# Kernel optimization log

Measured on AMD Instinct MI355X. Metric: run time of the kernel, lower is better.

The kernel has to match this reference:

```python
import jax, jax.numpy as jnp
import numpy as np

MODEL_DIM = 512
NUM_HEADS = 16
D_OUTPUT = 128
DIM_PER_HEAD = MODEL_DIM // NUM_HEADS  # 32
LN_EPS = 1e-5


def setup_inputs() -> dict:
    key = jax.random.key(0)
    ks = jax.random.split(key, 12)
    B = 128
    proj = MODEL_DIM * D_OUTPUT  # 65536
    s = 0.02
    return {
        "key": jax.random.normal(ks[0], (B, 1, MODEL_DIM), jnp.float32),
        "value": jax.random.normal(ks[1], (B, 1, MODEL_DIM), jnp.float32),
        "query": jax.random.normal(ks[2], (B, 1, MODEL_DIM), jnp.float32),
        "Wk": jax.random.normal(ks[3], (MODEL_DIM, proj), jnp.float32) * s,
        "bk": jnp.zeros((proj,), jnp.float32),
        "Wv": jax.random.normal(ks[4], (MODEL_DIM, proj), jnp.float32) * s,
        "bv": jnp.zeros((proj,), jnp.float32),
        "Wq": jax.random.normal(ks[5], (MODEL_DIM, proj), jnp.float32) * s,
        "bq": jnp.zeros((proj,), jnp.float32),
        "Wo": jax.random.normal(ks[6], (MODEL_DIM, MODEL_DIM), jnp.float32) * s,
        "bo": jnp.zeros((MODEL_DIM,), jnp.float32),
        "gamma": jnp.ones((MODEL_DIM,), jnp.float32),
        "beta": jnp.zeros((MODEL_DIM,), jnp.float32),
    }


def reference(key, value, query, Wk, bk, Wv, bv, Wq, bq, Wo, bo, gamma, beta):
    B = key.shape[0]
    residual = query  # [B, 1, model_dim]
    # QKV projections to model_dim*d_output, then view as (B*H, d_output, dim_per_head)
    k = (key @ Wk + bk).reshape(B * NUM_HEADS, -1, DIM_PER_HEAD)
    v = (value @ Wv + bv).reshape(B * NUM_HEADS, -1, DIM_PER_HEAD)
    q = (query @ Wq + bq).reshape(B * NUM_HEADS, -1, DIM_PER_HEAD)
    # faithful to original: scale = (dim_per_head // num_heads) ** -0.5 (int div)
    scale = (DIM_PER_HEAD // NUM_HEADS) ** (-0.5)
    scores = jnp.einsum('bqd,bkd->bqk', q, k) * scale  # [B*H, S, S]
    attn = jax.nn.softmax(scores, axis=2)
    context = jnp.einsum('bqk,bkd->bqd', attn, v)  # [B*H, S, dph]
    context = context.reshape(B, -1, DIM_PER_HEAD * NUM_HEADS)  # [B, d_output, model_dim]
    out = context @ Wo + bo
    x = residual + out  # broadcast [B,1,D] + [B,d_output,D]
    mu = jnp.mean(x, axis=-1, keepdims=True)
    var = jnp.mean(jnp.square(x - mu), axis=-1, keepdims=True)
    out = (x - mu) * jax.lax.rsqrt(var + LN_EPS) * gamma + beta
    return out, attn
```

## Files before the change

kernel.cpp:

```cpp
#include <hip/hip_runtime.h>

typedef unsigned short u16;
typedef unsigned int u32;
typedef __attribute__((ext_vector_type(4))) float f32x4;
typedef __attribute__((ext_vector_type(4))) u16 u16x4;
typedef __attribute__((ext_vector_type(8))) u16 u16x8;
typedef __attribute__((ext_vector_type(8))) __bf16 bf16x8;

#define DEV static __device__ __forceinline__

DEV u16 f2b(float f) {
  u32 u = __builtin_bit_cast(u32, f);
  u32 r = (u + 0x7fffu + ((u >> 16) & 1u)) >> 16;
  return (u16)r;
}

DEV bf16x8 mk8(u16x4 lo, u16x4 hi) {
  u16x8 v = __builtin_shufflevector(lo, hi, 0, 1, 2, 3, 4, 5, 6, 7);
  return __builtin_bit_cast(bf16x8, v);
}

__global__ __launch_bounds__(256) void prep_x(
    const float* __restrict__ key, const float* __restrict__ value,
    const float* __restrict__ query, u16* __restrict__ Xb)
{
  int idx = blockIdx.x * 256 + threadIdx.x;
  int mat = idx >> 14;
  int off = (idx & 16383) * 4;
  const float* src = mat == 0 ? key : (mat == 1 ? value : query);
  f32x4 v = *(const f32x4*)(src + off);
  u16x4 o;
#pragma unroll
  for (int i = 0; i < 4; ++i) o[i] = __builtin_bit_cast(u16, (__bf16)v[i]);
  *(u16x4*)(Xb + mat * 65536 + off) = o;
}

__global__ __launch_bounds__(256, 3) void qkv_gemm(
    const u16* __restrict__ Xb,
    const float* __restrict__ Wk, const float* __restrict__ bk,
    const float* __restrict__ Wv, const float* __restrict__ bv,
    const float* __restrict__ Wq, const float* __restrict__ bq,
    u16* __restrict__ Kp, u16* __restrict__ Vp, u16* __restrict__ Qp)
{
  const int bx = blockIdx.x;
  const int mat = bx >> 9;
  const float* W    = mat == 0 ? Wk : (mat == 1 ? Wv : Wq);
  const float* bias = mat == 0 ? bk : (mat == 1 ? bv : bq);
  u16* out          = mat == 0 ? Kp : (mat == 1 ? Vp : Qp);
  const u16* Xm = Xb + mat * 65536;
  const int n0 = (bx & 511) * 128;

  __shared__ float Bs[2][32 * 128];
  __shared__ u16   As[2][128 * 32];

  const int t0 = threadIdx.x, lane = t0 & 63, wv = t0 >> 6;
  const int wm = wv >> 1, wn = wv & 1;
  const int l15 = lane & 15, lg = lane >> 4;

  const int brow = wv * 8 + (lane >> 5);
  const int bcol = (lane & 31) * 4;

  f32x4 acc[4][4];
#pragma unroll
  for (int i = 0; i < 4; ++i)
#pragma unroll
    for (int j = 0; j < 4; ++j) acc[i][j] = (f32x4){0.f, 0.f, 0.f, 0.f};

  {
    f32x4 rB[4];
#pragma unroll
    for (int p = 0; p < 4; ++p) {
      int row = brow + p * 2;
      rB[p] = *(const f32x4*)(W + (size_t)row * 65536 + n0 + bcol);
    }
#pragma unroll
    for (int p = 0; p < 2; ++p) {
      int q = wv * 2 + p;
      int m = q * 16 + (lane >> 2);
      int sc = ((lane & 3) - ((m >> 1) & 3)) & 3;
      const u16* gp = Xm + m * 512 + sc * 8;
      u16* lp = &As[0][q * 512];
      __builtin_amdgcn_global_load_lds(
          (const __attribute__((address_space(1))) u32*)gp,
          (__attribute__((address_space(3))) u32*)lp, 16, 0, 0);
    }
#pragma unroll
    for (int p = 0; p < 4; ++p) {
      int row = brow + p * 2;
      int pc = (bcol + (((row >> 3) & 1) << 4)) & 127;
      *(f32x4*)&Bs[0][row * 128 + pc] = rB[p];
    }
    __syncthreads();
  }

  for (int t = 0; t < 16; ++t) {
    const int cur = t & 1, nxt = cur ^ 1;
    f32x4 rB[4];
    if (t < 15) {
      const int k0n = (t + 1) * 32;
#pragma unroll
      for (int p = 0; p < 4; ++p) {
        int row = brow + p * 2;
        rB[p] = *(const f32x4*)(W + (size_t)(k0n + row) * 65536 + n0 + bcol);
      }
#pragma unroll
      for (int p = 0; p < 2; ++p) {
        int q = wv * 2 + p;
        int m = q * 16 + (lane >> 2);
        int sc = ((lane & 3) - ((m >> 1) & 3)) & 3;
        const u16* gp = Xm + m * 512 + k0n + sc * 8;
        u16* lp = &As[nxt][q * 512];
        __builtin_amdgcn_global_load_lds(
            (const __attribute__((address_space(1))) u32*)gp,
            (__attribute__((address_space(3))) u32*)lp, 16, 0, 0);
      }
    }
    __builtin_amdgcn_sched_barrier(0);
    {
      bf16x8 af[4];
#pragma unroll
      for (int mf = 0; mf < 4; ++mf) {
        int m = wm * 64 + mf * 16 + l15;
        af[mf] = *(const bf16x8*)&As[cur][m * 32 + ((lg + ((m >> 1) & 3)) & 3) * 8];
      }
#pragma unroll
      for (int nf = 0; nf < 4; ++nf) {
        int pc = (wn * 64 + nf * 16 + l15 + ((lg & 1) << 4)) & 127;
        bf16x8 bv;
#pragma unroll
        for (int j = 0; j < 8; ++j) bv[j] = (__bf16)Bs[cur][(lg * 8 + j) * 128 + pc];
#pragma unroll
        for (int mf = 0; mf < 4; ++mf)
          acc[mf][nf] = __builtin_amdgcn_mfma_f32_16x16x32_bf16(af[mf], bv, acc[mf][nf], 0, 0, 0);
      }
    }
    __builtin_amdgcn_sched_barrier(0);
    if (t < 15) {
#pragma unroll
      for (int p = 0; p < 4; ++p) {
        int row = brow + p * 2;
        int pc = (bcol + (((row >> 3) & 1) << 4)) & 127;
        *(f32x4*)&Bs[nxt][row * 128 + pc] = rB[p];
      }
    }
    __syncthreads();
  }

  u16* tile = (u16*)&Bs[0][0];
#pragma unroll
  for (int nf = 0; nf < 4; ++nf) {
    int col = wn * 64 + nf * 16 + l15;
    float bv_ = bias[n0 + col];
#pragma unroll
    for (int mf = 0; mf < 4; ++mf) {
      int row0 = wm * 64 + mf * 16 + lg * 4;
#pragma unroll
      for (int r = 0; r < 4; ++r)
        tile[(row0 + r) * 128 + col] = f2b(acc[mf][nf][r] + bv_);
    }
  }
  __syncthreads();
#pragma unroll
  for (int rr = 0; rr < 16; ++rr) {
    int row = wv * 32 + rr * 2 + (lane >> 5);
    int c = (lane & 31) * 4;
    u16x4 v = *(const u16x4*)&tile[row * 128 + c];
    *(u16x4*)(out + (size_t)row * 65536 + n0 + c) = v;
  }
}

__global__ __launch_bounds__(256) void attn_kernel(
    const u16* __restrict__ Qp, const u16* __restrict__ Kp, const u16* __restrict__ Vp,
    float* __restrict__ attnOut, u16* __restrict__ ctx)
{
  const int bh = blockIdx.x;
  const int b = bh >> 4, h = bh & 15;
  const size_t base = (size_t)b * 65536 + h * 4096;

  __shared__ u16 qS[8 * 512];
  __shared__ u16 kS[8 * 512];
  __shared__ u16 vS[32 * 128];
  __shared__ u16 pS[32 * 512];

  const int t = threadIdx.x;
  const int lane = t & 63, w = t >> 6;
  const int l15 = lane & 15, lg = lane >> 4;

#pragma unroll
  for (int p = 0; p < 2; ++p) {
    int idx = p * 256 + t;
    int s = idx >> 2, dc = idx & 3;
    u16x8 qv = *(const u16x8*)(Qp + base + s * 32 + dc * 8);
    u16x8 kv = *(const u16x8*)(Kp + base + s * 32 + dc * 8);
    u16x8 vv = *(const u16x8*)(Vp + base + s * 32 + dc * 8);
    *(u16x4*)(qS + (dc * 2) * 512 + s * 4)     = __builtin_shufflevector(qv, qv, 0, 1, 2, 3);
    *(u16x4*)(qS + (dc * 2 + 1) * 512 + s * 4) = __builtin_shufflevector(qv, qv, 4, 5, 6, 7);
    *(u16x4*)(kS + (dc * 2) * 512 + s * 4)     = __builtin_shufflevector(kv, kv, 0, 1, 2, 3);
    *(u16x4*)(kS + (dc * 2 + 1) * 512 + s * 4) = __builtin_shufflevector(kv, kv, 4, 5, 6, 7);
#pragma unroll
    for (int i = 0; i < 8; ++i)
      vS[(s >> 2) * 128 + (dc * 8 + i) * 4 + (s & 3)] = vv[i];
  }
  __syncthreads();

  f32x4 sc[2][8];
#pragma unroll
  for (int i = 0; i < 2; ++i)
#pragma unroll
    for (int j = 0; j < 8; ++j) sc[i][j] = (f32x4){0.f, 0.f, 0.f, 0.f};

  {
    const int kqA = lg * 2;
    bf16x8 aq[2];
#pragma unroll
    for (int mf = 0; mf < 2; ++mf) {
      int m = w * 32 + mf * 16 + l15;
      u16x4 lo = *(const u16x4*)(qS + kqA * 512 + m * 4);
      u16x4 hi = *(const u16x4*)(qS + (kqA + 1) * 512 + m * 4);
      aq[mf] = mk8(lo, hi);
    }
#pragma unroll
    for (int nf = 0; nf < 8; ++nf) {
      int j = nf * 16 + l15;
      u16x4 lo = *(const u16x4*)(kS + kqA * 512 + j * 4);
      u16x4 hi = *(const u16x4*)(kS + (kqA + 1) * 512 + j * 4);
      bf16x8 bk8 = mk8(lo, hi);
#pragma unroll
      for (int mf = 0; mf < 2; ++mf)
        sc[mf][nf] = __builtin_amdgcn_mfma_f32_16x16x32_bf16(aq[mf], bk8, sc[mf][nf], 0, 0, 0);
    }
  }

  const float SCL = 0.70710678118654752f;
#pragma unroll
  for (int mf = 0; mf < 2; ++mf) {
#pragma unroll
    for (int r = 0; r < 4; ++r) {
      float m8 = -1e30f;
#pragma unroll
      for (int nf = 0; nf < 8; ++nf) m8 = fmaxf(m8, sc[mf][nf][r]);
      m8 = fmaxf(m8, __shfl_xor(m8, 1));
      m8 = fmaxf(m8, __shfl_xor(m8, 2));
      m8 = fmaxf(m8, __shfl_xor(m8, 4));
      m8 = fmaxf(m8, __shfl_xor(m8, 8));
      float s8 = 0.f;
#pragma unroll
      for (int nf = 0; nf < 8; ++nf) {
        float pv = __expf((sc[mf][nf][r] - m8) * SCL);
        sc[mf][nf][r] = pv;
        s8 += pv;
      }
      s8 += __shfl_xor(s8, 1);
      s8 += __shfl_xor(s8, 2);
      s8 += __shfl_xor(s8, 4);
      s8 += __shfl_xor(s8, 8);
      float inv = 1.0f / s8;
      int i = w * 32 + mf * 16 + lg * 4 + r;
      float* ao = attnOut + (size_t)bh * 16384 + (size_t)i * 128;
#pragma unroll
      for (int nf = 0; nf < 8; ++nf) {
        int j = nf * 16 + l15;
        float pv = sc[mf][nf][r] * inv;
        ao[j] = pv;
        pS[(j >> 2) * 512 + i * 4 + (j & 3)] = f2b(pv);
      }
    }
  }
  __syncthreads();

  f32x4 cacc[2][2];
#pragma unroll
  for (int i = 0; i < 2; ++i)
#pragma unroll
    for (int j = 0; j < 2; ++j) cacc[i][j] = (f32x4){0.f, 0.f, 0.f, 0.f};

#pragma unroll
  for (int ks2 = 0; ks2 < 4; ++ks2) {
    const int kqP = ks2 * 8 + lg * 2;
    bf16x8 ap[2];
#pragma unroll
    for (int mf = 0; mf < 2; ++mf) {
      int i = w * 32 + mf * 16 + l15;
      u16x4 lo = *(const u16x4*)(pS + kqP * 512 + i * 4);
      u16x4 hi = *(const u16x4*)(pS + (kqP + 1) * 512 + i * 4);
      ap[mf] = mk8(lo, hi);
    }
#pragma unroll
    for (int nf = 0; nf < 2; ++nf) {
      int d = nf * 16 + l15;
      u16x4 lo = *(const u16x4*)(vS + kqP * 128 + d * 4);
      u16x4 hi = *(const u16x4*)(vS + (kqP + 1) * 128 + d * 4);
      bf16x8 bv8 = mk8(lo, hi);
#pragma unroll
      for (int mf = 0; mf < 2; ++mf)
        cacc[mf][nf] = __builtin_amdgcn_mfma_f32_16x16x32_bf16(ap[mf], bv8, cacc[mf][nf], 0, 0, 0);
    }
  }

  __syncthreads();
#pragma unroll
  for (int mf = 0; mf < 2; ++mf) {
#pragma unroll
    for (int r = 0; r < 4; ++r) {
      int s = w * 32 + mf * 16 + lg * 4 + r;
      int p = s >> 4, q = s & 15;
#pragma unroll
      for (int nf = 0; nf < 2; ++nf) {
        int d = nf * 16 + l15;
        pS[p * 512 + q * 32 + d] = f2b(cacc[mf][nf][r]);
      }
    }
  }
#pragma unroll
  for (int pp = 0; pp < 2; ++pp) {
    int p = w * 2 + pp;
    u16x8 v = *(const u16x8*)&pS[p * 512 + lane * 8];
    *(u16x8*)(ctx + ((size_t)b * 128 + h * 8 + p) * 512 + lane * 8) = v;
  }
}

__global__ __launch_bounds__(256) void out_proj(
    const u16* __restrict__ ctx, const float* __restrict__ Wo, const float* __restrict__ bo,
    const float* __restrict__ query, float* __restrict__ pre)
{
  const int m0 = blockIdx.x * 128;
  const int n0 = blockIdx.y * 128;

  __shared__ u16 As[16 * 512];
  __shared__ u16 Bs[16 * 512];

  const int t = threadIdx.x;
  const int lane = t & 63, wid = t >> 6;
  const int wm = wid >> 1, wn = wid & 1;
  const int l15 = lane & 15, lg = lane >> 4;

  f32x4 acc[4][4];
#pragma unroll
  for (int i = 0; i < 4; ++i)
#pragma unroll
    for (int j = 0; j < 4; ++j) acc[i][j] = (f32x4){0.f, 0.f, 0.f, 0.f};

  for (int it = 0; it < 8; ++it) {
    const int k0 = it * 64;
#pragma unroll
    for (int p = 0; p < 4; ++p) {
      int idx = p * 256 + t;
      int m = idx >> 3, dc = idx & 7;
      u16x8 av = *(const u16x8*)(ctx + (size_t)(m0 + m) * 512 + k0 + dc * 8);
      int kq = dc * 2;
      *(u16x4*)(As + kq * 512 + (((m + 2 * kq) & 127) << 2)) =
          __builtin_shufflevector(av, av, 0, 1, 2, 3);
      *(u16x4*)(As + (kq + 1) * 512 + (((m + 2 * (kq + 1)) & 127) << 2)) =
          __builtin_shufflevector(av, av, 4, 5, 6, 7);
    }
#pragma unroll
    for (int p = 0; p < 8; ++p) {
      int idx = p * 256 + t;
      int n = idx & 127, kq = idx >> 7;
      const float* wp = Wo + (size_t)(k0 + kq * 4) * 512 + n0 + n;
      u16x4 uv;
      uv[0] = f2b(wp[0]);
      uv[1] = f2b(wp[512]);
      uv[2] = f2b(wp[1024]);
      uv[3] = f2b(wp[1536]);
      *(u16x4*)(Bs + kq * 512 + n * 4) = uv;
    }
    __syncthreads();
#pragma unroll
    for (int kstep = 0; kstep < 2; ++kstep) {
      const int kqA = kstep * 8 + lg * 2;
      bf16x8 af[4], bfr[4];
#pragma unroll
      for (int mf = 0; mf < 4; ++mf) {
        int m = wm * 64 + mf * 16 + l15;
        u16x4 lo = *(const u16x4*)(As + kqA * 512 + (((m + 2 * kqA) & 127) << 2));
        u16x4 hi = *(const u16x4*)(As + (kqA + 1) * 512 + (((m + 2 * (kqA + 1)) & 127) << 2));
        af[mf] = mk8(lo, hi);
      }
#pragma unroll
      for (int nf = 0; nf < 4; ++nf) {
        int n = wn * 64 + nf * 16 + l15;
        u16x4 lo = *(const u16x4*)(Bs + kqA * 512 + n * 4);
        u16x4 hi = *(const u16x4*)(Bs + (kqA + 1) * 512 + n * 4);
        bfr[nf] = mk8(lo, hi);
      }
#pragma unroll
      for (int mf = 0; mf < 4; ++mf)
#pragma unroll
        for (int nf = 0; nf < 4; ++nf)
          acc[mf][nf] = __builtin_amdgcn_mfma_f32_16x16x32_bf16(af[mf], bfr[nf], acc[mf][nf], 0, 0, 0);
    }
    __syncthreads();
  }

#pragma unroll
  for (int nf = 0; nf < 4; ++nf) {
    int col = wn * 64 + nf * 16 + l15;
    float bv_ = bo[n0 + col];
#pragma unroll
    for (int mf = 0; mf < 4; ++mf) {
      int row0 = wm * 64 + mf * 16 + lg * 4;
#pragma unroll
      for (int r = 0; r < 4; ++r) {
        int m = m0 + row0 + r;
        float res = query[(m >> 7) * 512 + n0 + col];
        pre[(size_t)m * 512 + n0 + col] = acc[mf][nf][r] + bv_ + res;
      }
    }
  }
}

__global__ __launch_bounds__(256) void ln_kernel(
    const float* __restrict__ pre, const float* __restrict__ gamma,
    const float* __restrict__ beta, float* __restrict__ out0)
{
  const int w = threadIdx.x >> 6, lane = threadIdx.x & 63;
  const int row = blockIdx.x * 4 + w;
  const float* x = pre + (size_t)row * 512;
  f32x4 v0 = *(const f32x4*)(x + lane * 8);
  f32x4 v1 = *(const f32x4*)(x + lane * 8 + 4);
  float s = v0[0] + v0[1] + v0[2] + v0[3] + v1[0] + v1[1] + v1[2] + v1[3];
  float q = v0[0] * v0[0] + v0[1] * v0[1] + v0[2] * v0[2] + v0[3] * v0[3] +
            v1[0] * v1[0] + v1[1] * v1[1] + v1[2] * v1[2] + v1[3] * v1[3];
#pragma unroll
  for (int m = 1; m < 64; m <<= 1) {
    s += __shfl_xor(s, m);
    q += __shfl_xor(q, m);
  }
  float mean = s * (1.f / 512.f);
  float var = q * (1.f / 512.f) - mean * mean;
  float rs = rsqrtf(var + 1e-5f);
  f32x4 g0 = *(const f32x4*)(gamma + lane * 8);
  f32x4 g1 = *(const f32x4*)(gamma + lane * 8 + 4);
  f32x4 b0 = *(const f32x4*)(beta + lane * 8);
  f32x4 b1 = *(const f32x4*)(beta + lane * 8 + 4);
  f32x4 o0, o1;
#pragma unroll
  for (int i = 0; i < 4; ++i) {
    o0[i] = (v0[i] - mean) * rs * g0[i] + b0[i];
    o1[i] = (v1[i] - mean) * rs * g1[i] + b1[i];
  }
  *(f32x4*)(out0 + (size_t)row * 512 + lane * 8) = o0;
  *(f32x4*)(out0 + (size_t)row * 512 + lane * 8 + 4) = o1;
}

extern "C" void kernel_launch(void* const* d_in, const int* in_sizes, int n_in,
                              void* d_out, int out_size, void* d_ws, size_t ws_size,
                              hipStream_t stream) {
  (void)in_sizes; (void)n_in; (void)out_size; (void)ws_size;
  const float* key   = (const float*)d_in[0];
  const float* value = (const float*)d_in[1];
  const float* query = (const float*)d_in[2];
  const float* Wk    = (const float*)d_in[3];
  const float* bk    = (const float*)d_in[4];
  const float* Wv    = (const float*)d_in[5];
  const float* bv    = (const float*)d_in[6];
  const float* Wq    = (const float*)d_in[7];
  const float* bq    = (const float*)d_in[8];
  const float* Wo    = (const float*)d_in[9];
  const float* bo    = (const float*)d_in[10];
  const float* gamma = (const float*)d_in[11];
  const float* beta  = (const float*)d_in[12];

  char* ws = (char*)d_ws;
  u16* Kp  = (u16*)(ws + 0);
  u16* Vp  = (u16*)(ws + 16777216);
  u16* Qp  = (u16*)(ws + 33554432);
  u16* ctx = (u16*)(ws + 50331648);
  u16* Xb  = (u16*)(ws + 50331648);
  float* pre = (float*)(ws + 0);

  float* out0    = (float*)d_out;
  float* attnOut = out0 + 8388608;

  prep_x<<<dim3(192), 256, 0, stream>>>(key, value, query, Xb);
  qkv_gemm<<<dim3(1536), 256, 0, stream>>>(Xb, Wk, bk, Wv, bv, Wq, bq, Kp, Vp, Qp);
  attn_kernel<<<dim3(2048), 256, 0, stream>>>(Qp, Kp, Vp, attnOut, ctx);
  out_proj<<<dim3(128, 4), 256, 0, stream>>>(ctx, Wo, bo, query, pre);
  ln_kernel<<<dim3(4096), 256, 0, stream>>>(pre, gamma, beta, out0);
}
```

Before: 192.0 us.

## Fuse output projection with LayerNorm and pre-convert Wo to bf16 layout

Replaces the separate out_proj and ln_kernel with one kernel in which each block computes 32 full 512-wide rows, adds bias and residual, and applies LayerNorm in registers using a cross-wave LDS reduction. This removes the fp32 round trip of the pre-norm activations through global memory. A small wo_prep kernel converts Wo once to a bf16 k-quad layout, which the fused kernel streams into LDS with global_load_lds. A-fragments are read straight from global. The trade-offs are fewer blocks (512) with a whole 512-column B tile per iteration, plus one extra launch.

```diff
diff --git a/kernel.cpp b/kernel.cpp
--- a/kernel.cpp
+++ b/kernel.cpp
@@ -319,129 +319,118 @@
   }
 }
 
-__global__ __launch_bounds__(256) void out_proj(
-    const u16* __restrict__ ctx, const float* __restrict__ Wo, const float* __restrict__ bo,
-    const float* __restrict__ query, float* __restrict__ pre)
+__global__ __launch_bounds__(256) void wo_prep(
+    const float* __restrict__ Wo, u16* __restrict__ Wot)
 {
-  const int m0 = blockIdx.x * 128;
-  const int n0 = blockIdx.y * 128;
-
-  __shared__ u16 As[16 * 512];
-  __shared__ u16 Bs[16 * 512];
-
-  const int t = threadIdx.x;
-  const int lane = t & 63, wid = t >> 6;
-  const int wm = wid >> 1, wn = wid & 1;
+  int idx = blockIdx.x * 256 + threadIdx.x;
+  int k = idx >> 7;
+  int n = (idx & 127) * 4;
+  f32x4 v = *(const f32x4*)(Wo + k * 512 + n);
+  int kq = k >> 2, j = k & 3;
+#pragma unroll
+  for (int i = 0; i < 4; ++i)
+    Wot[kq * 2048 + (n + i) * 4 + j] = f2b(v[i]);
+}
+
+__global__ __launch_bounds__(256) void fused_out_ln(
+    const u16* __restrict__ ctx, const u16* __restrict__ Wot,
+    const float* __restrict__ bo, const float* __restrict__ query,
+    const float* __restrict__ gamma, const float* __restrict__ beta,
+    float* __restrict__ out0)
+{
+  const int bid = blockIdx.x;
+  const int m0 = bid * 32;
+  const int b = bid >> 2;
+  const int t = threadIdx.x, lane = t & 63, wv = t >> 6;
   const int l15 = lane & 15, lg = lane >> 4;
-
-  f32x4 acc[4][4];
-#pragma unroll
-  for (int i = 0; i < 4; ++i)
-#pragma unroll
-    for (int j = 0; j < 4; ++j) acc[i][j] = (f32x4){0.f, 0.f, 0.f, 0.f};
-
-  for (int it = 0; it < 8; ++it) {
-    const int k0 = it * 64;
-#pragma unroll
-    for (int p = 0; p < 4; ++p) {
-      int idx = p * 256 + t;
-      int m = idx >> 3, dc = idx & 7;
-      u16x8 av = *(const u16x8*)(ctx + (size_t)(m0 + m) * 512 + k0 + dc * 8);
-      int kq = dc * 2;
-      *(u16x4*)(As + kq * 512 + (((m + 2 * kq) & 127) << 2)) =
-          __builtin_shufflevector(av, av, 0, 1, 2, 3);
-      *(u16x4*)(As + (kq + 1) * 512 + (((m + 2 * (kq + 1)) & 127) << 2)) =
-          __builtin_shufflevector(av, av, 4, 5, 6, 7);
-    }
+  const int qb = wv * 128;
+
+  __shared__ u16 Bs2[8 * 512 * 4];
+  __shared__ float redS[128], redQ[128];
+
+  f32x4 acc[2][8];
+#pragma unroll
+  for (int i = 0; i < 2; ++i)
+#pragma unroll
+    for (int j = 0; j < 8; ++j) acc[i][j] = (f32x4){0.f, 0.f, 0.f, 0.f};
+
+  for (int it = 0; it < 16; ++it) {
 #pragma unroll
     for (int p = 0; p < 8; ++p) {
-      int idx = p * 256 + t;
-      int n = idx & 127, kq = idx >> 7;
-      const float* wp = Wo + (size_t)(k0 + kq * 4) * 512 + n0 + n;
-      u16x4 uv;
-      uv[0] = f2b(wp[0]);
-      uv[1] = f2b(wp[512]);
-      uv[2] = f2b(wp[1024]);
-      uv[3] = f2b(wp[1536]);
-      *(u16x4*)(Bs + kq * 512 + n * 4) = uv;
-    }
+      int q = wv * 8 + p;
+      const u16* gp = Wot + it * 16384 + q * 512 + lane * 8;
+      u16* lp = Bs2 + q * 512;
+      __builtin_amdgcn_global_load_lds(
+          (const __attribute__((address_space(1))) u32*)gp,
+          (__attribute__((address_space(3))) u32*)lp, 16, 0, 0);
+    }
+    bf16x8 af[2];
+#pragma unroll
+    for (int mf = 0; mf < 2; ++mf)
+      af[mf] = *(const bf16x8*)(ctx + (size_t)(m0 + mf * 16 + l15) * 512 + it * 32 + lg * 8);
     __syncthreads();
 #pragma unroll
-    for (int kstep = 0; kstep < 2; ++kstep) {
-      const int kqA = kstep * 8 + lg * 2;
-      bf16x8 af[4], bfr[4];
-#pragma unroll
-      for (int mf = 0; mf < 4; ++mf) {
-        int m = wm * 64 + mf * 16 + l15;
-        u16x4 lo = *(const u16x4*)(As + kqA * 512 + (((m + 2 * kqA) & 127) << 2));
-        u16x4 hi = *(const u16x4*)(As + (kqA + 1) * 512 + (((m + 2 * (kqA + 1)) & 127) << 2));
-        af[mf] = mk8(lo, hi);
-      }
-#pragma unroll
-      for (int nf = 0; nf < 4; ++nf) {
-        int n = wn * 64 + nf * 16 + l15;
-        u16x4 lo = *(const u16x4*)(Bs + kqA * 512 + n * 4);
-        u16x4 hi = *(const u16x4*)(Bs + (kqA + 1) * 512 + n * 4);
-        bfr[nf] = mk8(lo, hi);
-      }
-#pragma unroll
-      for (int mf = 0; mf < 4; ++mf)
-#pragma unroll
-        for (int nf = 0; nf < 4; ++nf)
-          acc[mf][nf] = __builtin_amdgcn_mfma_f32_16x16x32_bf16(af[mf], bfr[nf], acc[mf][nf], 0, 0, 0);
+    for (int nf = 0; nf < 8; ++nf) {
+      int n = qb + nf * 16 + l15;
+      u16x4 lo = *(const u16x4*)(Bs2 + (2 * lg) * 2048 + n * 4);
+      u16x4 hi = *(const u16x4*)(Bs2 + (2 * lg + 1) * 2048 + n * 4);
+      bf16x8 bfr = mk8(lo, hi);
+      acc[0][nf] = __builtin_amdgcn_mfma_f32_16x16x32_bf16(af[0], bfr, acc[0][nf], 0, 0, 0);
+      acc[1][nf] = __builtin_amdgcn_mfma_f32_16x16x32_bf16(af[1], bfr, acc[1][nf], 0, 0, 0);
     }
     __syncthreads();
   }
 
-#pragma unroll
-  for (int nf = 0; nf < 4; ++nf) {
-    int col = wn * 64 + nf * 16 + l15;
-    float bv_ = bo[n0 + col];
-#pragma unroll
-    for (int mf = 0; mf < 4; ++mf) {
-      int row0 = wm * 64 + mf * 16 + lg * 4;
-#pragma unroll
-      for (int r = 0; r < 4; ++r) {
-        int m = m0 + row0 + r;
-        float res = query[(m >> 7) * 512 + n0 + col];
-        pre[(size_t)m * 512 + n0 + col] = acc[mf][nf][r] + bv_ + res;
-      }
-    }
-  }
-}
-
-__global__ __launch_bounds__(256) void ln_kernel(
-    const float* __restrict__ pre, const float* __restrict__ gamma,
-    const float* __restrict__ beta, float* __restrict__ out0)
-{
-  const int w = threadIdx.x >> 6, lane = threadIdx.x & 63;
-  const int row = blockIdx.x * 4 + w;
-  const float* x = pre + (size_t)row * 512;
-  f32x4 v0 = *(const f32x4*)(x + lane * 8);
-  f32x4 v1 = *(const f32x4*)(x + lane * 8 + 4);
-  float s = v0[0] + v0[1] + v0[2] + v0[3] + v1[0] + v1[1] + v1[2] + v1[3];
-  float q = v0[0] * v0[0] + v0[1] * v0[1] + v0[2] * v0[2] + v0[3] * v0[3] +
-            v1[0] * v1[0] + v1[1] * v1[1] + v1[2] * v1[2] + v1[3] * v1[3];
-#pragma unroll
-  for (int m = 1; m < 64; m <<= 1) {
-    s += __shfl_xor(s, m);
-    q += __shfl_xor(q, m);
-  }
-  float mean = s * (1.f / 512.f);
-  float var = q * (1.f / 512.f) - mean * mean;
-  float rs = rsqrtf(var + 1e-5f);
-  f32x4 g0 = *(const f32x4*)(gamma + lane * 8);
-  f32x4 g1 = *(const f32x4*)(gamma + lane * 8 + 4);
-  f32x4 b0 = *(const f32x4*)(beta + lane * 8);
-  f32x4 b1 = *(const f32x4*)(beta + lane * 8 + 4);
-  f32x4 o0, o1;
-#pragma unroll
-  for (int i = 0; i < 4; ++i) {
-    o0[i] = (v0[i] - mean) * rs * g0[i] + b0[i];
-    o1[i] = (v1[i] - mean) * rs * g1[i] + b1[i];
-  }
-  *(f32x4*)(out0 + (size_t)row * 512 + lane * 8) = o0;
-  *(f32x4*)(out0 + (size_t)row * 512 + lane * 8 + 4) = o1;
+  float bo8[8], qr8[8], g8[8], be8[8];
+#pragma unroll
+  for (int nf = 0; nf < 8; ++nf) {
+    int col = qb + nf * 16 + l15;
+    bo8[nf] = bo[col];
+    qr8[nf] = query[b * 512 + col];
+    g8[nf] = gamma[col];
+    be8[nf] = beta[col];
+  }
+#pragma unroll
+  for (int mf = 0; mf < 2; ++mf)
+#pragma unroll
+    for (int nf = 0; nf < 8; ++nf)
+#pragma unroll
+      for (int r = 0; r < 4; ++r)
+        acc[mf][nf][r] += bo8[nf] + qr8[nf];
+
+#pragma unroll
+  for (int mf = 0; mf < 2; ++mf)
+#pragma unroll
+    for (int r = 0; r < 4; ++r) {
+      float s = 0.f, q2 = 0.f;
+#pragma unroll
+      for (int nf = 0; nf < 8; ++nf) {
+        float x = acc[mf][nf][r];
+        s += x; q2 += x * x;
+      }
+      s += __shfl_xor(s, 1);  s += __shfl_xor(s, 2);
+      s += __shfl_xor(s, 4);  s += __shfl_xor(s, 8);
+      q2 += __shfl_xor(q2, 1); q2 += __shfl_xor(q2, 2);
+      q2 += __shfl_xor(q2, 4); q2 += __shfl_xor(q2, 8);
+      int row = mf * 16 + lg * 4 + r;
+      if (l15 == 0) { redS[wv * 32 + row] = s; redQ[wv * 32 + row] = q2; }
+    }
+  __syncthreads();
+#pragma unroll
+  for (int mf = 0; mf < 2; ++mf)
+#pragma unroll
+    for (int r = 0; r < 4; ++r) {
+      int row = mf * 16 + lg * 4 + r;
+      float s = redS[row] + redS[32 + row] + redS[64 + row] + redS[96 + row];
+      float q2 = redQ[row] + redQ[32 + row] + redQ[64 + row] + redQ[96 + row];
+      float mean = s * (1.f / 512.f);
+      float var = q2 * (1.f / 512.f) - mean * mean;
+      float rs = rsqrtf(var + 1e-5f);
+#pragma unroll
+      for (int nf = 0; nf < 8; ++nf)
+        out0[(size_t)(m0 + row) * 512 + qb + nf * 16 + l15] =
+            (acc[mf][nf][r] - mean) * rs * g8[nf] + be8[nf];
+    }
 }
 
 extern "C" void kernel_launch(void* const* d_in, const int* in_sizes, int n_in,
@@ -468,7 +457,7 @@
   u16* Qp  = (u16*)(ws + 33554432);
   u16* ctx = (u16*)(ws + 50331648);
   u16* Xb  = (u16*)(ws + 50331648);
-  float* pre = (float*)(ws + 0);
+  u16* Wot = (u16*)(ws + 0);
 
   float* out0    = (float*)d_out;
   float* attnOut = out0 + 8388608;
@@ -476,6 +465,6 @@
   prep_x<<<dim3(192), 256, 0, stream>>>(key, value, query, Xb);
   qkv_gemm<<<dim3(1536), 256, 0, stream>>>(Xb, Wk, bk, Wv, bv, Wq, bq, Kp, Vp, Qp);
   attn_kernel<<<dim3(2048), 256, 0, stream>>>(Qp, Kp, Vp, attnOut, ctx);
-  out_proj<<<dim3(128, 4), 256, 0, stream>>>(ctx, Wo, bo, query, pre);
-  ln_kernel<<<dim3(4096), 256, 0, stream>>>(pre, gamma, beta, out0);
-}
+  wo_prep<<<dim3(256), 256, 0, stream>>>(Wo, Wot);
+  fused_out_ln<<<dim3(512), 256, 0, stream>>>(ctx, Wot, bo, query, gamma, beta, out0);
+}
```

Result: faster. 186.6 us (-2.8%).
